# Optimization experiments

Hardware: AMD Instinct MI355X
Metric: run time of the kernel (lower is better)

The kernel has to match this reference:

```python
import jax, jax.numpy as jnp
import numpy as np

B, T, D = 1, 4096, 2048
NUM_HEADS, NUM_KV_HEADS, HEAD_DIM = 16, 8, 128
QUERY_PRE_ATTN_SCALAR = HEAD_DIM ** -0.5
SOFT_CAP = 50.0
WINDOW = 1024
ROPE_BASE = 10000.0
ROPE_SCALE = 1.0
K_MASK = -2.3819763e+38


def apply_rope(x, positions, head_dim, max_wavelength=ROPE_BASE, scale_factor=ROPE_SCALE):
    # x: [B, T, N, H], positions: [B, T]
    fraction = 2.0 * jnp.arange(head_dim // 2, dtype=jnp.float32) / head_dim
    timescale = max_wavelength ** fraction  # [H/2]
    sinusoid = positions[..., None].astype(jnp.float32) / timescale  # [B, T, H/2]
    sinusoid = (sinusoid / scale_factor)[..., None, :]  # [B, T, 1, H/2]
    sin, cos = jnp.sin(sinusoid), jnp.cos(sinusoid)
    first, second = jnp.split(x, 2, axis=-1)
    out = jnp.concatenate([first * cos - second * sin,
                           second * cos + first * sin], axis=-1)
    return out.astype(x.dtype)


def setup_inputs() -> dict:
    key = jax.random.key(0)
    ks = jax.random.split(key, 4)
    x = jax.random.normal(ks[0], (B, T, D), dtype=jnp.float32)
    segment_pos = jnp.broadcast_to(jnp.arange(T, dtype=jnp.int32), (B, T))
    # causal mask [B, T, S]
    attn_mask = jnp.broadcast_to(
        jnp.tril(jnp.ones((T, T), dtype=jnp.bool_)), (B, T, T))
    q_w = jax.random.normal(ks[1], (NUM_HEADS, D, HEAD_DIM), dtype=jnp.float32) * 0.02
    kv_w = jax.random.normal(ks[2], (2, NUM_KV_HEADS, D, HEAD_DIM), dtype=jnp.float32) * 0.02
    o_w = jax.random.normal(ks[3], (NUM_HEADS, HEAD_DIM, D), dtype=jnp.float32) * 0.02
    return {"x": x, "segment_pos": segment_pos, "attn_mask": attn_mask,
            "q_w": q_w, "kv_w": kv_w, "o_w": o_w}


def reference(x, segment_pos, attn_mask, q_w, kv_w, o_w):
    # Projections (GQA: separate q and kv einsums)
    q = jnp.einsum('BTD,NDH->BTNH', x, q_w)          # [B,T,N,H]
    k = jnp.einsum('BSD,KDH->BSKH', x, kv_w[0])      # [B,S,K,H]
    v = jnp.einsum('BSD,KDH->BSKH', x, kv_w[1])      # [B,S,K,H]

    q = apply_rope(q, segment_pos, HEAD_DIM)
    q = q * QUERY_PRE_ATTN_SCALAR
    k = apply_rope(k, segment_pos, HEAD_DIM)

    num_groups = NUM_HEADS // NUM_KV_HEADS
    qg = q.reshape(B, T, NUM_KV_HEADS, num_groups, HEAD_DIM)
    logits = jnp.einsum('BTKGH,BSKH->BTKGS', qg, k)
    logits = logits.reshape(B, T, NUM_HEADS, -1)     # [B,T,N,S]

    # soft cap
    logits = jnp.tanh(logits / SOFT_CAP) * SOFT_CAP

    # sliding-window mask combined with causal mask
    all_ones = jnp.ones_like(attn_mask)
    sliding = jnp.triu(all_ones, -WINDOW + 1) * jnp.tril(all_ones, WINDOW - 1)
    mask = sliding * attn_mask                       # [B,T,S] bool

    padded = jnp.where(mask[:, :, None, :], logits, K_MASK)
    probs = jax.nn.softmax(padded, axis=-1).astype(k.dtype)

    probs_g = probs.reshape(B, T, NUM_KV_HEADS, num_groups, -1)
    encoded = jnp.einsum('BTKGS,BSKH->BTKGH', probs_g, v)
    encoded = encoded.reshape(B, T, NUM_HEADS, HEAD_DIM)

    attn_output = jnp.einsum('BTNH,NHD->BTD', encoded, o_w)
    return attn_output
```

## Files before the change

### kernel.cpp

```cpp
#include <hip/hip_runtime.h>
#include <hip/hip_bf16.h>
#include <math.h>

typedef __attribute__((ext_vector_type(8))) short short8;
typedef __attribute__((ext_vector_type(8))) unsigned short ushort8;
typedef __attribute__((ext_vector_type(4))) float f32x4;
typedef __attribute__((ext_vector_type(2))) float f32x2;

#define T_SEQ 4096
#define D_MODEL 2048
#define N_HEADS 16
#define N_KV 8
#define HEAD_DIM 128
#define QSCALE 0.08838834764831845f

__device__ __forceinline__ float bf2f(unsigned short u) {
  union { unsigned int i; float f; } x; x.i = ((unsigned int)u) << 16; return x.f;
}
__device__ __forceinline__ unsigned short f2bf(float f) {
  union { float f; unsigned int i; } x; x.f = f;
  unsigned int i = x.i;
  unsigned int r = i + 0x7fffu + ((i >> 16) & 1u);
  return (unsigned short)(r >> 16);
}

__global__ __launch_bounds__(256) void prep_kernel(const float* __restrict__ x,
                                                   unsigned short* __restrict__ xb,
                                                   const int* __restrict__ segpos,
                                                   float2* __restrict__ tab) {
  int b = blockIdx.x;
  if (b < 4096) {
    int idx = b * 256 + threadIdx.x;
    const float4* p = reinterpret_cast<const float4*>(x) + (size_t)idx * 2;
    float4 a = p[0], c = p[1];
    ushort8 o;
    o[0] = f2bf(a.x); o[1] = f2bf(a.y); o[2] = f2bf(a.z); o[3] = f2bf(a.w);
    o[4] = f2bf(c.x); o[5] = f2bf(c.y); o[6] = f2bf(c.z); o[7] = f2bf(c.w);
    reinterpret_cast<ushort8*>(xb)[idx] = o;
  } else {
    int idx = (b - 4096) * 256 + threadIdx.x;
    int t = idx >> 6, i = idx & 63;
    float pos = (float)segpos[t];
    float ts = powf(10000.f, (float)(2 * i) / 128.f);
    float ang = pos / ts;
    tab[idx] = make_float2(sinf(ang), cosf(ang));
  }
}

__global__ __launch_bounds__(256) void wqkv_transpose_kernel(const float* __restrict__ q_w,
                                                             const float* __restrict__ kv_w,
                                                             unsigned short* __restrict__ Wt) {
  __shared__ float tile[32][33];
  int z = blockIdx.z;
  const float* src = (z < 16) ? q_w + (size_t)z * 2048 * 128
                              : kv_w + (size_t)(z - 16) * 2048 * 128;
  unsigned short* dst = Wt + (size_t)z * 128 * 2048;
  int c0 = blockIdx.x * 32, r0 = blockIdx.y * 32;
  int tx = threadIdx.x & 31, ty = threadIdx.x >> 5;
#pragma unroll
  for (int i = 0; i < 4; ++i)
    tile[ty + i * 8][tx] = src[(size_t)(r0 + ty + i * 8) * 128 + c0 + tx];
  __syncthreads();
#pragma unroll
  for (int i = 0; i < 4; ++i)
    dst[(size_t)(c0 + ty + i * 8) * 2048 + r0 + tx] = f2bf(tile[tx][ty + i * 8]);
}

#define G2L(gp, lp)                                                           \
  __builtin_amdgcn_global_load_lds(                                           \
      (const __attribute__((address_space(1))) void*)(gp),                    \
      (__attribute__((address_space(3))) void*)(lp), 16, 0, 0)
#define GBAR() asm volatile("s_barrier" ::: "memory")
#define VMW(n) asm volatile("s_waitcnt vmcnt(" #n ")" ::: "memory")
#define LG0()  asm volatile("s_waitcnt lgkmcnt(0)" ::: "memory")

template <int OUT_BF16>
__global__ __launch_bounds__(512, 2) void gemm256_kernel(const unsigned short* __restrict__ A,
                                                         const unsigned short* __restrict__ Bt,
                                                         void* __restrict__ Cout,
                                                         int M, int N, int K) {
  extern __shared__ unsigned short smem[];
  unsigned short* ldsA = smem;
  unsigned short* ldsB = smem + 32768;
  const int tid = threadIdx.x;
  const int lane = tid & 63, wave = tid >> 6;
  const int wm = wave >> 2, wn = wave & 3;
  const int lr = lane & 15, lg = lane >> 4;
  const int swz = (lr & 7) << 3;
  const int c0s = (lg * 8) ^ swz;
  const int c1s = (32 + lg * 8) ^ swz;

  int id = blockIdx.y * gridDim.x + blockIdx.x;
  int nb = gridDim.x * gridDim.y;
  int sw = (id & 7) * (nb >> 3) + (id >> 3);
  const long brow = (long)(sw / gridDim.x) * 256;
  const long bcol = (long)(sw % gridDim.x) * 256;

  const unsigned short* Ag = A + brow * K;
  const unsigned short* Bg = Bt + bcol * K;

  const int r0 = tid >> 3;
  const int cs = ((tid & 7) * 8) ^ ((r0 & 7) << 3);

#define ST_A(tt, b, a)                                                        \
  { G2L(Ag + (size_t)((a) * 128 + r0) * K + (size_t)(tt) * 64 + cs,           \
        ldsA + (b) * 16384 + (a) * 8192 + tid * 8);                           \
    G2L(Ag + (size_t)((a) * 128 + r0 + 64) * K + (size_t)(tt) * 64 + cs,      \
        ldsA + (b) * 16384 + (a) * 8192 + 4096 + tid * 8); }
#define ST_B(tt, b, h)                                                        \
  { G2L(Bg + (size_t)((h) * 128 + r0) * K + (size_t)(tt) * 64 + cs,           \
        ldsB + (b) * 16384 + (h) * 8192 + tid * 8);                           \
    G2L(Bg + (size_t)((h) * 128 + r0 + 64) * K + (size_t)(tt) * 64 + cs,      \
        ldsB + (b) * 16384 + (h) * 8192 + 4096 + tid * 8); }

  f32x4 acc[8][4] = {};
  short8 bf[4][2];
  short8 af[4];

#define RD_B(b)                                                               \
  { const unsigned short* pb = ldsB + (b) * 16384 + wn * 4096;                \
    _Pragma("unroll")                                                         \
    for (int n = 0; n < 4; ++n) {                                             \
      bf[n][0] = *(const short8*)(pb + (n * 16 + lr) * 64 + c0s);             \
      bf[n][1] = *(const short8*)(pb + (n * 16 + lr) * 64 + c1s);             \
    } }
#define RD_A(b, mb)                                                           \
  { const unsigned short* pa = ldsA + (b) * 16384 + wm * 8192;                \
    af[0] = *(const short8*)(pa + ((mb) * 16 + lr) * 64 + c0s);               \
    af[1] = *(const short8*)(pa + ((mb) * 16 + lr) * 64 + c1s);               \
    af[2] = *(const short8*)(pa + ((mb) * 16 + 16 + lr) * 64 + c0s);          \
    af[3] = *(const short8*)(pa + ((mb) * 16 + 16 + lr) * 64 + c1s); }
#define MFMA2(mb)                                                             \
  { __builtin_amdgcn_s_setprio(1);                                            \
    _Pragma("unroll")                                                         \
    for (int n = 0; n < 4; ++n) {                                             \
      acc[mb][n]     = __builtin_amdgcn_mfma_f32_16x16x32_bf16(af[0], bf[n][0], acc[mb][n], 0, 0, 0);     \
      acc[mb][n]     = __builtin_amdgcn_mfma_f32_16x16x32_bf16(af[1], bf[n][1], acc[mb][n], 0, 0, 0);     \
      acc[mb + 1][n] = __builtin_amdgcn_mfma_f32_16x16x32_bf16(af[2], bf[n][0], acc[mb + 1][n], 0, 0, 0); \
      acc[mb + 1][n] = __builtin_amdgcn_mfma_f32_16x16x32_bf16(af[3], bf[n][1], acc[mb + 1][n], 0, 0, 0); \
    }                                                                         \
    __builtin_amdgcn_s_setprio(0); }

  const int NT = K >> 6;
  ST_B(0, 0, 0); ST_B(0, 0, 1); ST_A(0, 0, 0); ST_A(0, 0, 1);
  ST_B(1, 1, 0); ST_B(1, 1, 1);
  VMW(4); GBAR();
  for (int j = 0; j < (NT >> 1); ++j) {
    const int c1 = 2 * j + 1, t2 = 2 * j + 2, t3 = 2 * j + 3;
    const bool s2 = t2 < NT, s3 = t3 < NT;
    RD_B(0); RD_A(0, 0); ST_A(c1, 1, 0);
    GBAR(); LG0(); MFMA2(0); GBAR();
    RD_A(0, 2); ST_A(c1, 1, 1);
    if (s2) ST_B(t2, 0, 0);
    GBAR(); MFMA2(2); GBAR();
    RD_A(0, 4);
    if (s2) ST_B(t2, 0, 1);
    GBAR(); MFMA2(4); GBAR();
    RD_A(0, 6);
    if (s2) { VMW(4); } else { VMW(0); }
    GBAR(); LG0(); MFMA2(6); GBAR();
    RD_B(1); RD_A(1, 0);
    if (s2) ST_A(t2, 0, 0);
    GBAR(); LG0(); MFMA2(0); GBAR();
    RD_A(1, 2);
    if (s2) ST_A(t2, 0, 1);
    if (s3) ST_B(t3, 1, 0);
    GBAR(); MFMA2(2); GBAR();
    RD_A(1, 4);
    if (s3) ST_B(t3, 1, 1);
    GBAR(); MFMA2(4); GBAR();
    RD_A(1, 6);
    if (s3) { VMW(4); } else { VMW(0); }
    GBAR(); LG0(); MFMA2(6); GBAR();
  }

#pragma unroll
  for (int m = 0; m < 8; ++m) {
#pragma unroll
    for (int i = 0; i < 4; ++i) {
      long row = brow + wm * 128 + m * 16 + lg * 4 + i;
#pragma unroll
      for (int n = 0; n < 4; ++n) {
        long col = bcol + wn * 64 + n * 16 + lr;
        if (OUT_BF16)
          ((unsigned short*)Cout)[row * N + col] = f2bf(acc[m][n][i]);
        else
          ((float*)Cout)[row * N + col] = acc[m][n][i];
      }
    }
  }
#undef ST_A
#undef ST_B
#undef RD_A
#undef RD_B
#undef MFMA2
}

__global__ __launch_bounds__(512, 1) void gemm_op3_kernel(const unsigned short* __restrict__ A,
                                                          const unsigned short* __restrict__ Bt,
                                                          float* __restrict__ Cout,
                                                          int M, int N, int K) {
  extern __shared__ unsigned short smem[];
  unsigned short* ldsA = smem;
  unsigned short* ldsB = smem + 3 * 8192;
  const int tid = threadIdx.x;
  const int lane = tid & 63, wave = tid >> 6;
  const int wm = wave >> 2, wn = wave & 3;
  const int lr = lane & 15, lg = lane >> 4;
  const int swz = (lr & 7) << 3;
  const int c0s = (lg * 8) ^ swz;
  const int c1s = (32 + lg * 8) ^ swz;

  int id = blockIdx.y * gridDim.x + blockIdx.x;
  int sw = (id & 7) * 32 + (id >> 3);
  int c = sw >> 5, l = sw & 31;
  const long brow = (long)((c >> 2) * 16 + (l & 15)) * 128;
  const long bcol = (long)((c & 3) * 2 + (l >> 4)) * 256;

  const unsigned short* Ag = A + brow * K;
  const unsigned short* Bg = Bt + bcol * K;

  const int r0 = tid >> 3;
  const int cs = ((tid & 7) * 8) ^ ((r0 & 7) << 3);

#define ST_A3(tt, b)                                                          \
  { G2L(Ag + (size_t)(r0) * K + (size_t)(tt) * 64 + cs,                       \
        ldsA + (b) * 8192 + tid * 8);                                         \
    G2L(Ag + (size_t)(r0 + 64) * K + (size_t)(tt) * 64 + cs,                  \
        ldsA + (b) * 8192 + 4096 + tid * 8); }
#define ST_B3(tt, b, h)                                                       \
  { G2L(Bg + (size_t)((h) * 128 + r0) * K + (size_t)(tt) * 64 + cs,           \
        ldsB + (b) * 16384 + (h) * 8192 + tid * 8);                           \
    G2L(Bg + (size_t)((h) * 128 + r0 + 64) * K + (size_t)(tt) * 64 + cs,      \
        ldsB + (b) * 16384 + (h) * 8192 + 4096 + tid * 8); }

  f32x4 acc[4][4] = {};
  short8 bf[4][2];
  short8 af[4];

#define RD_B3(b)                                                              \
  { const unsigned short* pb = ldsB + (b) * 16384 + wn * 4096;                \
    _Pragma("unroll")                                                         \
    for (int n = 0; n < 4; ++n) {                                             \
      bf[n][0] = *(const short8*)(pb + (n * 16 + lr) * 64 + c0s);             \
      bf[n][1] = *(const short8*)(pb + (n * 16 + lr) * 64 + c1s);             \
    } }
#define RD_A3(b, mb)                                                          \
  { const unsigned short* pa = ldsA + (b) * 8192 + wm * 4096;                 \
    af[0] = *(const short8*)(pa + ((mb) * 16 + lr) * 64 + c0s);               \
    af[1] = *(const short8*)(pa + ((mb) * 16 + lr) * 64 + c1s);               \
    af[2] = *(const short8*)(pa + ((mb) * 16 + 16 + lr) * 64 + c0s);          \
    af[3] = *(const short8*)(pa + ((mb) * 16 + 16 + lr) * 64 + c1s); }
#define MFMA2(mb)                                                             \
  { __builtin_amdgcn_s_setprio(1);                                            \
    _Pragma("unroll")                                                         \
    for (int n = 0; n < 4; ++n) {                                             \
      acc[mb][n]     = __builtin_amdgcn_mfma_f32_16x16x32_bf16(af[0], bf[n][0], acc[mb][n], 0, 0, 0);     \
      acc[mb][n]     = __builtin_amdgcn_mfma_f32_16x16x32_bf16(af[1], bf[n][1], acc[mb][n], 0, 0, 0);     \
      acc[mb + 1][n] = __builtin_amdgcn_mfma_f32_16x16x32_bf16(af[2], bf[n][0], acc[mb + 1][n], 0, 0, 0); \
      acc[mb + 1][n] = __builtin_amdgcn_mfma_f32_16x16x32_bf16(af[3], bf[n][1], acc[mb + 1][n], 0, 0, 0); \
    }                                                                         \
    __builtin_amdgcn_s_setprio(0); }

  const int NT = K >> 6;
  ST_B3(0, 0, 0); ST_B3(0, 0, 1); ST_A3(0, 0);
  ST_B3(1, 1, 0); ST_B3(1, 1, 1); ST_A3(1, 1);
  VMW(6); GBAR();
  int b = 0;
  for (int t = 0; t < NT; ++t) {
    int bn = b + 2; if (bn >= 3) bn -= 3;
    const bool st = (t + 2) < NT;
    RD_B3(b); RD_A3(b, 0);
    if (st) { ST_B3(t + 2, bn, 0); ST_B3(t + 2, bn, 1); }
    GBAR(); LG0(); MFMA2(0); GBAR();
    RD_A3(b, 2);
    if (st) { ST_A3(t + 2, bn); VMW(6); } else { VMW(0); }
    GBAR(); LG0(); MFMA2(2); GBAR();
    b = b + 1; if (b >= 3) b = 0;
  }

#pragma unroll
  for (int m = 0; m < 4; ++m) {
#pragma unroll
    for (int i = 0; i < 4; ++i) {
      long row = brow + wm * 64 + m * 16 + lg * 4 + i;
#pragma unroll
      for (int n = 0; n < 4; ++n) {
        long col = bcol + wn * 64 + n * 16 + lr;
        Cout[row * N + col] = acc[m][n][i];
      }
    }
  }
#undef ST_A3
#undef ST_B3
#undef RD_A3
#undef RD_B3
#undef MFMA2
}

__global__ __launch_bounds__(256) void rope_vt_ow_kernel(const unsigned short* __restrict__ raw,
                                                         const float2* __restrict__ tab,
                                                         unsigned short* __restrict__ Qb,
                                                         unsigned short* __restrict__ Kb,
                                                         unsigned short* __restrict__ Vt,
                                                         const float* __restrict__ o_w,
                                                         unsigned short* __restrict__ o_wt) {
  __shared__ unsigned short tileU[32][33];
  __shared__ float tileF[32][33];
  int b = blockIdx.x;
  if (b < 3072) {
    int gid = b * 256 + threadIdx.x;
    int j = gid & 7;
    int rem = gid >> 3;
    int hs = rem % 24;
    int t = rem / 24;
    int i0 = j * 8;
    float sv[8], cv[8];
    const float2* tp = tab + t * 64 + i0;
#pragma unroll
    for (int q = 0; q < 8; ++q) { float2 sc2 = tp[q]; sv[q] = sc2.x; cv[q] = sc2.y; }
    if (hs < 16) {
      const unsigned short* p = raw + (size_t)t * 4096 + hs * 128 + i0;
      ushort8 a = *(const ushort8*)p;
      ushort8 c = *(const ushort8*)(p + 64);
      ushort8 o1, o2;
#pragma unroll
      for (int q = 0; q < 8; ++q) {
        float fa = bf2f(a[q]), fb = bf2f(c[q]);
        o1[q] = f2bf((fa * cv[q] - fb * sv[q]) * QSCALE);
        o2[q] = f2bf((fb * cv[q] + fa * sv[q]) * QSCALE);
      }
      unsigned short* qp = Qb + ((size_t)hs * T_SEQ + t) * 128 + i0;
      *(ushort8*)qp = o1;
      *(ushort8*)(qp + 64) = o2;
    } else {
      int kn = hs - 16;
      const unsigned short* p = raw + (size_t)t * 4096 + 2048 + kn * 128 + i0;
      ushort8 a = *(const ushort8*)p;
      ushort8 c = *(const ushort8*)(p + 64);
      ushort8 o1, o2;
#pragma unroll
      for (int q = 0; q < 8; ++q) {
        float fa = bf2f(a[q]), fb = bf2f(c[q]);
        o1[q] = f2bf(fa * cv[q] - fb * sv[q]);
        o2[q] = f2bf(fb * cv[q] + fa * sv[q]);
      }
      unsigned short* kp = Kb + ((size_t)kn * T_SEQ + t) * 128 + i0;
      *(ushort8*)kp = o1;
      *(ushort8*)(kp + 64) = o2;
    }
  } else if (b < 7168) {
    int id = b - 3072;
    int bx = id & 3, by = (id >> 2) & 127, bz = id >> 9;
    const unsigned short* src = raw + 3072 + (size_t)bz * 128;
    unsigned short* dst = Vt + (size_t)bz * 128 * 4096;
    int c0 = bx * 32, r0 = by * 32;
    int tx = threadIdx.x & 31, ty = threadIdx.x >> 5;
#pragma unroll
    for (int i = 0; i < 4; ++i)
      tileU[ty + i * 8][tx] = src[(size_t)(r0 + ty + i * 8) * 4096 + c0 + tx];
    __syncthreads();
#pragma unroll
    for (int i = 0; i < 4; ++i)
      dst[(size_t)(c0 + ty + i * 8) * 4096 + r0 + tx] = tileU[tx][ty + i * 8];
  } else {
    int id = b - 7168;
    int bx = id & 63, by = id >> 6;
    int c0 = bx * 32, r0 = by * 32;
    int tx = threadIdx.x & 31, ty = threadIdx.x >> 5;
#pragma unroll
    for (int i = 0; i < 4; ++i)
      tileF[ty + i * 8][tx] = o_w[(size_t)(r0 + ty + i * 8) * 2048 + c0 + tx];
    __syncthreads();
#pragma unroll
    for (int i = 0; i < 4; ++i)
      o_wt[(size_t)(c0 + ty + i * 8) * 2048 + r0 + tx] = f2bf(tileF[tx][ty + i * 8]);
  }
}

__global__ __launch_bounds__(512, 2) void attn_kernel(const unsigned short* __restrict__ Qb,
                                                      const unsigned short* __restrict__ Kb,
                                                      const unsigned short* __restrict__ Vt,
                                                      unsigned short* __restrict__ enc) {
  __shared__ unsigned short Ks[2][64][128];
  __shared__ unsigned short Vs[2][128][64];
  __shared__ unsigned short Ps[8][32][72];
  int rawb = blockIdx.x;
  int lin = (rawb & 7) * 32 + (rawb >> 3);
  const int h = lin >> 4;
  const int qb0 = (lin & 15) * 256;
  const int kvh = h >> 1;
  const int tid = threadIdx.x, lane = tid & 63, wave = tid >> 6;
  const int qw = qb0 + wave * 32;
  const int lr = lane & 15, lg = lane >> 4;
  const int sw = (lr & 7) << 3;
  const int ck0 = (lg * 8) ^ sw, ck1 = (32 + lg * 8) ^ sw;
  const int ck2 = (64 + lg * 8) ^ sw, ck3 = (96 + lg * 8) ^ sw;

  short8 aq[2][4];
#pragma unroll
  for (int g = 0; g < 2; ++g) {
    const unsigned short* qp = Qb + ((size_t)h * T_SEQ + qw + g * 16 + lr) * 128 + lg * 8;
#pragma unroll
    for (int c = 0; c < 4; ++c) aq[g][c] = *(const short8*)(qp + c * 32);
  }
  f32x4 acc[2][8] = {};
  float lsum[2] = {0.f, 0.f};

  const int s_lo = (qb0 - 1023) > 0 ? (qb0 - 1023) : 0;
  const int kb_lo = s_lo >> 6, kb_hi = (qb0 + 255) >> 6;

  const int rK = tid >> 4;
  const int cpK = (tid & 15) * 8;
  const int colK = cpK ^ ((rK & 7) << 3);
  const int rV = tid >> 3;
  const int cpV = (tid & 7) * 8;
  const int colV = cpV ^ ((rV & 7) << 3);
  const unsigned short* kgb = Kb + ((size_t)kvh * T_SEQ + rK) * 128 + colK;
  const unsigned short* vgb = Vt + ((size_t)kvh * 128 + rV) * T_SEQ + colV;

  ushort8 kr0, kr1, vr0, vr1;
  {
    const int s0g = kb_lo * 64;
    kr0 = *(const ushort8*)(kgb + (size_t)s0g * 128);
    kr1 = *(const ushort8*)(kgb + (size_t)(s0g + 32) * 128);
    vr0 = *(const ushort8*)(vgb + s0g);
    vr1 = *(const ushort8*)(vgb + (size_t)64 * T_SEQ + s0g);
  }

  const int qg0 = qw + lr, qg1 = qw + 16 + lr;
  for (int kb = kb_lo; kb <= kb_hi; ++kb) {
    const int s0g = kb * 64;
    const int buf = kb & 1;
    *(ushort8*)&Ks[buf][rK][cpK] = kr0;
    *(ushort8*)&Ks[buf][rK + 32][cpK] = kr1;
    *(ushort8*)&Vs[buf][rV][cpV] = vr0;
    *(ushort8*)&Vs[buf][rV + 64][cpV] = vr1;
    __syncthreads();
    if (kb < kb_hi) {
      const int sn = s0g + 64;
      kr0 = *(const ushort8*)(kgb + (size_t)sn * 128);
      kr1 = *(const ushort8*)(kgb + (size_t)(sn + 32) * 128);
      vr0 = *(const ushort8*)(vgb + sn);
      vr1 = *(const ushort8*)(vgb + (size_t)64 * T_SEQ + sn);
    }
    if (s0g > qw + 31 || s0g + 63 < qw - 1023) continue;
    const bool interior = (s0g + 63 <= qw) && (s0g >= qw - 992);

    f32x4 sT0[4] = {}, sT1[4] = {};
    __builtin_amdgcn_s_setprio(1);
#pragma unroll
    for (int st = 0; st < 4; ++st) {
      const unsigned short* kp = &Ks[buf][st * 16 + lr][0];
      short8 k0 = *(const short8*)(kp + ck0);
      short8 k1 = *(const short8*)(kp + ck1);
      short8 k2 = *(const short8*)(kp + ck2);
      short8 k3 = *(const short8*)(kp + ck3);
      sT0[st] = __builtin_amdgcn_mfma_f32_16x16x32_bf16(k0, aq[0][0], sT0[st], 0, 0, 0);
      sT1[st] = __builtin_amdgcn_mfma_f32_16x16x32_bf16(k0, aq[1][0], sT1[st], 0, 0, 0);
      sT0[st] = __builtin_amdgcn_mfma_f32_16x16x32_bf16(k1, aq[0][1], sT0[st], 0, 0, 0);
      sT1[st] = __builtin_amdgcn_mfma_f32_16x16x32_bf16(k1, aq[1][1], sT1[st], 0, 0, 0);
      sT0[st] = __builtin_amdgcn_mfma_f32_16x16x32_bf16(k2, aq[0][2], sT0[st], 0, 0, 0);
      sT1[st] = __builtin_amdgcn_mfma_f32_16x16x32_bf16(k2, aq[1][2], sT1[st], 0, 0, 0);
      sT0[st] = __builtin_amdgcn_mfma_f32_16x16x32_bf16(k3, aq[0][3], sT0[st], 0, 0, 0);
      sT1[st] = __builtin_amdgcn_mfma_f32_16x16x32_bf16(k3, aq[1][3], sT1[st], 0, 0, 0);
    }
    __builtin_amdgcn_s_setprio(0);

#pragma unroll
    for (int g = 0; g < 2; ++g) {
      const f32x4* sTg = g ? sT1 : sT0;
      const int qgg = g ? qg1 : qg0;
#pragma unroll
      for (int st = 0; st < 4; ++st) {
        f32x4 svv = sTg[st];
        f32x2 sa, sb;
        sa[0] = svv[0]; sa[1] = svv[1]; sb[0] = svv[2]; sb[1] = svv[3];
        f32x2 ua = sa * sa, ub = sb * sb;
        f32x2 numa = ua * 4.0e-4f + 15.f, numb = ub * 4.0e-4f + 15.f;
        f32x2 dena = ua * 2.4e-3f + 15.f, denb = ub * 2.4e-3f + 15.f;
        f32x2 ra, rb;
        ra[0] = __builtin_amdgcn_rcpf(dena[0]); ra[1] = __builtin_amdgcn_rcpf(dena[1]);
        rb[0] = __builtin_amdgcn_rcpf(denb[0]); rb[1] = __builtin_amdgcn_rcpf(denb[1]);
        f32x2 ea = (sa * 1.44269504f) * numa * ra;
        f32x2 eb = (sb * 1.44269504f) * numb * rb;
        float e[4] = {ea[0], ea[1], eb[0], eb[1]};
        float p[4];
#pragma unroll
        for (int r = 0; r < 4; ++r) {
          if (!interior) {
            int sg = s0g + st * 16 + lg * 4 + r;
            e[r] = ((unsigned)(qgg - sg) <= 1023u) ? e[r] : -__builtin_inff();
          }
          asm("v_exp_f32 %0, %1" : "=v"(p[r]) : "v"(e[r]));
        }
        lsum[g] += (p[0] + p[1]) + (p[2] + p[3]);
        unsigned u0, u1;
        asm("v_cvt_pk_bf16_f32 %0, %1, %2" : "=v"(u0) : "v"(p[0]), "v"(p[1]));
        asm("v_cvt_pk_bf16_f32 %0, %1, %2" : "=v"(u1) : "v"(p[2]), "v"(p[3]));
        uint2 w; w.x = u0; w.y = u1;
        *(uint2*)&Ps[wave][g * 16 + lr][st * 16 + lg * 4] = w;
      }
    }
    short8 pa00 = *(const short8*)&Ps[wave][lr][lg * 8];
    short8 pa01 = *(const short8*)&Ps[wave][lr][32 + lg * 8];
    short8 pa10 = *(const short8*)&Ps[wave][16 + lr][lg * 8];
    short8 pa11 = *(const short8*)&Ps[wave][16 + lr][32 + lg * 8];
    __builtin_amdgcn_s_setprio(1);
#pragma unroll
    for (int d0 = 0; d0 < 8; ++d0) {
      const unsigned short* vp = &Vs[buf][d0 * 16 + lr][0];
      short8 bv0 = *(const short8*)(vp + ((lg * 8) ^ sw));
      short8 bv1 = *(const short8*)(vp + ((32 + lg * 8) ^ sw));
      acc[0][d0] = __builtin_amdgcn_mfma_f32_16x16x32_bf16(pa00, bv0, acc[0][d0], 0, 0, 0);
      acc[1][d0] = __builtin_amdgcn_mfma_f32_16x16x32_bf16(pa10, bv0, acc[1][d0], 0, 0, 0);
      acc[0][d0] = __builtin_amdgcn_mfma_f32_16x16x32_bf16(pa01, bv1, acc[0][d0], 0, 0, 0);
      acc[1][d0] = __builtin_amdgcn_mfma_f32_16x16x32_bf16(pa11, bv1, acc[1][d0], 0, 0, 0);
    }
    __builtin_amdgcn_s_setprio(0);
  }

#pragma unroll
  for (int g = 0; g < 2; ++g) {
    float l = lsum[g];
    l += __shfl_xor(l, 16);
    l += __shfl_xor(l, 32);
#pragma unroll
    for (int r = 0; r < 4; ++r) {
      float lt = __shfl(l, lg * 4 + r);
      float inv = __builtin_amdgcn_rcpf(lt);
      int row = qw + g * 16 + lg * 4 + r;
      unsigned short* op = enc + (size_t)row * D_MODEL + h * 128 + lr;
#pragma unroll
      for (int d0 = 0; d0 < 8; ++d0) op[d0 * 16] = f2bf(acc[g][d0][r] * inv);
    }
  }
}

extern "C" void kernel_launch(void* const* d_in, const int* in_sizes, int n_in,
                              void* d_out, int out_size, void* d_ws, size_t ws_size,
                              hipStream_t stream) {
  const float* x = (const float*)d_in[0];
  const int* segpos = (const int*)d_in[1];
  const float* q_w = (const float*)d_in[3];
  const float* kv_w = (const float*)d_in[4];
  const float* o_w = (const float*)d_in[5];
  float* out = (float*)d_out;
  char* ws = (char*)d_ws;

  const size_t OFF_XB = 0;
  const size_t OFF_WT = OFF_XB + 16777216;
  const size_t OFF_RAW = OFF_WT + 16777216;
  const size_t OFF_KB = OFF_RAW + 33554432;
  const size_t OFF_VT = OFF_KB + 8388608;
  const size_t OFF_TAB = OFF_VT + 8388608;
  unsigned short* xb = (unsigned short*)(ws + OFF_XB);
  unsigned short* Wt = (unsigned short*)(ws + OFF_WT);
  unsigned short* raw = (unsigned short*)(ws + OFF_RAW);
  unsigned short* Kb = (unsigned short*)(ws + OFF_KB);
  unsigned short* Vt = (unsigned short*)(ws + OFF_VT);
  float2* tab = (float2*)(ws + OFF_TAB);
  unsigned short* o_wt = xb;
  unsigned short* Qb = Wt;
  unsigned short* enc = raw;

  hipFuncSetAttribute((const void*)(gemm256_kernel<1>),
                      hipFuncAttributeMaxDynamicSharedMemorySize, 131072);
  hipFuncSetAttribute((const void*)gemm_op3_kernel,
                      hipFuncAttributeMaxDynamicSharedMemorySize, 147456);

  prep_kernel<<<dim3(5120), dim3(256), 0, stream>>>(x, xb, segpos, tab);
  wqkv_transpose_kernel<<<dim3(4, 64, 32), dim3(256), 0, stream>>>(q_w, kv_w, Wt);
  gemm256_kernel<1><<<dim3(16, 16), dim3(512), 131072, stream>>>(xb, Wt, (void*)raw, 4096, 4096, 2048);
  rope_vt_ow_kernel<<<dim3(11264), dim3(256), 0, stream>>>(raw, tab, Qb, Kb, Vt, o_w, o_wt);
  attn_kernel<<<dim3(256), dim3(512), 0, stream>>>(Qb, Kb, Vt, enc);
  gemm_op3_kernel<<<dim3(8, 32), dim3(512), 147456, stream>>>(enc, o_wt, out, 4096, 2048, 2048);
}
```

Baseline: 200.5 us.

## Retile output-projection GEMM to 256x128 tiles with double buffering and two blocks/CU

```diff
diff --git a/kernel.cpp b/kernel.cpp
--- a/kernel.cpp
+++ b/kernel.cpp
@@ -196,13 +196,13 @@
 #undef MFMA2
 }
 
-__global__ __launch_bounds__(512, 1) void gemm_op3_kernel(const unsigned short* __restrict__ A,
-                                                          const unsigned short* __restrict__ Bt,
-                                                          float* __restrict__ Cout,
-                                                          int M, int N, int K) {
+__global__ __launch_bounds__(512, 2) void gemm_ob_kernel(const unsigned short* __restrict__ A,
+                                                         const unsigned short* __restrict__ Bt,
+                                                         float* __restrict__ Cout,
+                                                         int M, int N, int K) {
   extern __shared__ unsigned short smem[];
   unsigned short* ldsA = smem;
-  unsigned short* ldsB = smem + 3 * 8192;
+  unsigned short* ldsB = smem + 32768;
   const int tid = threadIdx.x;
   const int lane = tid & 63, wave = tid >> 6;
   const int wm = wave >> 2, wn = wave & 3;
@@ -212,10 +212,10 @@
   const int c1s = (32 + lg * 8) ^ swz;
 
   int id = blockIdx.y * gridDim.x + blockIdx.x;
-  int sw = (id & 7) * 32 + (id >> 3);
-  int c = sw >> 5, l = sw & 31;
-  const long brow = (long)((c >> 2) * 16 + (l & 15)) * 128;
-  const long bcol = (long)((c & 3) * 2 + (l >> 4)) * 256;
+  int nb = gridDim.x * gridDim.y;
+  int sw = (id & 7) * (nb >> 3) + (id >> 3);
+  const long brow = (long)(sw / gridDim.x) * 256;
+  const long bcol = (long)(sw % gridDim.x) * 128;
 
   const unsigned short* Ag = A + brow * K;
   const unsigned short* Bg = Bt + bcol * K;
@@ -223,30 +223,30 @@
   const int r0 = tid >> 3;
   const int cs = ((tid & 7) * 8) ^ ((r0 & 7) << 3);
 
-#define ST_A3(tt, b)                                                          \
-  { G2L(Ag + (size_t)(r0) * K + (size_t)(tt) * 64 + cs,                       \
-        ldsA + (b) * 8192 + tid * 8);                                         \
-    G2L(Ag + (size_t)(r0 + 64) * K + (size_t)(tt) * 64 + cs,                  \
-        ldsA + (b) * 8192 + 4096 + tid * 8); }
-#define ST_B3(tt, b, h)                                                       \
-  { G2L(Bg + (size_t)((h) * 128 + r0) * K + (size_t)(tt) * 64 + cs,           \
-        ldsB + (b) * 16384 + (h) * 8192 + tid * 8);                           \
-    G2L(Bg + (size_t)((h) * 128 + r0 + 64) * K + (size_t)(tt) * 64 + cs,      \
-        ldsB + (b) * 16384 + (h) * 8192 + 4096 + tid * 8); }
-
-  f32x4 acc[4][4] = {};
-  short8 bf[4][2];
+#define ST_A(tt, b, a)                                                        \
+  { G2L(Ag + (size_t)((a) * 128 + r0) * K + (size_t)(tt) * 64 + cs,           \
+        ldsA + (b) * 16384 + (a) * 8192 + tid * 8);                           \
+    G2L(Ag + (size_t)((a) * 128 + r0 + 64) * K + (size_t)(tt) * 64 + cs,      \
+        ldsA + (b) * 16384 + (a) * 8192 + 4096 + tid * 8); }
+#define ST_B(tt, b)                                                           \
+  { G2L(Bg + (size_t)(r0) * K + (size_t)(tt) * 64 + cs,                       \
+        ldsB + (b) * 8192 + tid * 8);                                         \
+    G2L(Bg + (size_t)(r0 + 64) * K + (size_t)(tt) * 64 + cs,                  \
+        ldsB + (b) * 8192 + 4096 + tid * 8); }
+
+  f32x4 acc[8][2] = {};
+  short8 bf[2][2];
   short8 af[4];
 
-#define RD_B3(b)                                                              \
-  { const unsigned short* pb = ldsB + (b) * 16384 + wn * 4096;                \
+#define RD_B(b)                                                               \
+  { const unsigned short* pb = ldsB + (b) * 8192 + wn * 2048;                 \
     _Pragma("unroll")                                                         \
-    for (int n = 0; n < 4; ++n) {                                             \
+    for (int n = 0; n < 2; ++n) {                                             \
       bf[n][0] = *(const short8*)(pb + (n * 16 + lr) * 64 + c0s);             \
       bf[n][1] = *(const short8*)(pb + (n * 16 + lr) * 64 + c1s);             \
     } }
-#define RD_A3(b, mb)                                                          \
-  { const unsigned short* pa = ldsA + (b) * 8192 + wm * 4096;                 \
+#define RD_A(b, mb)                                                           \
+  { const unsigned short* pa = ldsA + (b) * 16384 + wm * 8192;                \
     af[0] = *(const short8*)(pa + ((mb) * 16 + lr) * 64 + c0s);               \
     af[1] = *(const short8*)(pa + ((mb) * 16 + lr) * 64 + c1s);               \
     af[2] = *(const short8*)(pa + ((mb) * 16 + 16 + lr) * 64 + c0s);          \
@@ -254,7 +254,7 @@
 #define MFMA2(mb)                                                             \
   { __builtin_amdgcn_s_setprio(1);                                            \
     _Pragma("unroll")                                                         \
-    for (int n = 0; n < 4; ++n) {                                             \
+    for (int n = 0; n < 2; ++n) {                                             \
       acc[mb][n]     = __builtin_amdgcn_mfma_f32_16x16x32_bf16(af[0], bf[n][0], acc[mb][n], 0, 0, 0);     \
       acc[mb][n]     = __builtin_amdgcn_mfma_f32_16x16x32_bf16(af[1], bf[n][1], acc[mb][n], 0, 0, 0);     \
       acc[mb + 1][n] = __builtin_amdgcn_mfma_f32_16x16x32_bf16(af[2], bf[n][0], acc[mb + 1][n], 0, 0, 0); \
@@ -263,38 +263,52 @@
     __builtin_amdgcn_s_setprio(0); }
 
   const int NT = K >> 6;
-  ST_B3(0, 0, 0); ST_B3(0, 0, 1); ST_A3(0, 0);
-  ST_B3(1, 1, 0); ST_B3(1, 1, 1); ST_A3(1, 1);
-  VMW(6); GBAR();
-  int b = 0;
-  for (int t = 0; t < NT; ++t) {
-    int bn = b + 2; if (bn >= 3) bn -= 3;
-    const bool st = (t + 2) < NT;
-    RD_B3(b); RD_A3(b, 0);
-    if (st) { ST_B3(t + 2, bn, 0); ST_B3(t + 2, bn, 1); }
+  ST_B(0, 0); ST_A(0, 0, 0); ST_A(0, 0, 1);
+  ST_B(1, 1);
+  VMW(2); GBAR();
+  for (int j = 0; j < (NT >> 1); ++j) {
+    const int c1 = 2 * j + 1, t2 = 2 * j + 2, t3 = 2 * j + 3;
+    const bool s2 = t2 < NT, s3 = t3 < NT;
+    RD_B(0); RD_A(0, 0); ST_A(c1, 1, 0);
     GBAR(); LG0(); MFMA2(0); GBAR();
-    RD_A3(b, 2);
-    if (st) { ST_A3(t + 2, bn); VMW(6); } else { VMW(0); }
-    GBAR(); LG0(); MFMA2(2); GBAR();
-    b = b + 1; if (b >= 3) b = 0;
-  }
-
-#pragma unroll
-  for (int m = 0; m < 4; ++m) {
+    RD_A(0, 2); ST_A(c1, 1, 1);
+    if (s2) ST_B(t2, 0);
+    GBAR(); MFMA2(2); GBAR();
+    RD_A(0, 4);
+    GBAR(); MFMA2(4); GBAR();
+    RD_A(0, 6);
+    if (s2) { VMW(2); } else { VMW(0); }
+    GBAR(); LG0(); MFMA2(6); GBAR();
+    RD_B(1); RD_A(1, 0);
+    if (s2) ST_A(t2, 0, 0);
+    GBAR(); LG0(); MFMA2(0); GBAR();
+    RD_A(1, 2);
+    if (s2) ST_A(t2, 0, 1);
+    if (s3) ST_B(t3, 1);
+    GBAR(); MFMA2(2); GBAR();
+    RD_A(1, 4);
+    GBAR(); MFMA2(4); GBAR();
+    RD_A(1, 6);
+    if (s3) { VMW(2); } else { VMW(0); }
+    GBAR(); LG0(); MFMA2(6); GBAR();
+  }
+
+#pragma unroll
+  for (int m = 0; m < 8; ++m) {
 #pragma unroll
     for (int i = 0; i < 4; ++i) {
-      long row = brow + wm * 64 + m * 16 + lg * 4 + i;
-#pragma unroll
-      for (int n = 0; n < 4; ++n) {
-        long col = bcol + wn * 64 + n * 16 + lr;
+      long row = brow + wm * 128 + m * 16 + lg * 4 + i;
+#pragma unroll
+      for (int n = 0; n < 2; ++n) {
+        long col = bcol + wn * 32 + n * 16 + lr;
         Cout[row * N + col] = acc[m][n][i];
       }
     }
   }
-#undef ST_A3
-#undef ST_B3
-#undef RD_A3
-#undef RD_B3
+#undef ST_A
+#undef ST_B
+#undef RD_A
+#undef RD_B
 #undef MFMA2
 }
 
@@ -566,13 +580,13 @@
 
   hipFuncSetAttribute((const void*)(gemm256_kernel<1>),
                       hipFuncAttributeMaxDynamicSharedMemorySize, 131072);
-  hipFuncSetAttribute((const void*)gemm_op3_kernel,
-                      hipFuncAttributeMaxDynamicSharedMemorySize, 147456);
+  hipFuncSetAttribute((const void*)gemm_ob_kernel,
+                      hipFuncAttributeMaxDynamicSharedMemorySize, 98304);
 
   prep_kernel<<<dim3(5120), dim3(256), 0, stream>>>(x, xb, segpos, tab);
   wqkv_transpose_kernel<<<dim3(4, 64, 32), dim3(256), 0, stream>>>(q_w, kv_w, Wt);
   gemm256_kernel<1><<<dim3(16, 16), dim3(512), 131072, stream>>>(xb, Wt, (void*)raw, 4096, 4096, 2048);
   rope_vt_ow_kernel<<<dim3(11264), dim3(256), 0, stream>>>(raw, tab, Qb, Kb, Vt, o_w, o_wt);
   attn_kernel<<<dim3(256), dim3(512), 0, stream>>>(Qb, Kb, Vt, enc);
-  gemm_op3_kernel<<<dim3(8, 32), dim3(512), 147456, stream>>>(enc, o_wt, out, 4096, 2048, 2048);
-}
+  gemm_ob_kernel<<<dim3(16, 16), dim3(512), 98304, stream>>>(enc, o_wt, out, 4096, 2048, 2048);
+}
```

After: 197.5 us. Within noise of the previous version (-1.5%).
